# Performance work log

Measured on AMD Instinct MI355X. Metric: run time of the kernel, lower is better.

## Reference

```python
import jax, jax.numpy as jnp
import numpy as np

B, CIN, H, W = 32, 10, 128, 128
APP, WIDTH, M1, M2 = 2, 64, 20, 20
NQ, NP, OUT, MID = 4, 2, 1, 128
LIFT = WIDTH - CIN - APP - NQ  # 48


def setup_inputs() -> dict:
    key = jax.random.key(0)
    ks = jax.random.split(key, 16)
    n = lambda k, s: jax.random.normal(k, s, dtype=jnp.float32)
    sc = 1.0 / (WIDTH * WIDTH)  # FNO spectral weight scale 1/(in*out)
    return {
        'x': n(ks[0], (B, CIN, H, W)),
        'qa': n(ks[1], (NQ, CIN + APP)) * 0.1,
        'qb': n(ks[2], (NQ, CIN + APP)) * 0.1,
        'fc0_w1': n(ks[3], (MID, CIN + APP + NQ)) * 0.1,
        'fc0_b1': jnp.zeros((MID,), jnp.float32),
        'fc0_w2': n(ks[4], (LIFT, MID)) * 0.1,
        'fc0_b2': jnp.zeros((LIFT,), jnp.float32),
        'sw1r': n(ks[5], (4, WIDTH, WIDTH, M1, M2)) * sc,
        'sw1i': n(ks[6], (4, WIDTH, WIDTH, M1, M2)) * sc,
        'sw2r': n(ks[7], (4, WIDTH, WIDTH, M1, M2)) * sc,
        'sw2i': n(ks[8], (4, WIDTH, WIDTH, M1, M2)) * sc,
        'cw': n(ks[9], (4, WIDTH, WIDTH, 3, 3)) * 0.05,
        'cb': jnp.zeros((4, WIDTH), jnp.float32),
        'pw': n(ks[10], (4, WIDTH, 2 * WIDTH + NP)) * 0.05,
        'pb': jnp.zeros((4, WIDTH), jnp.float32),
        'fc1_w1': n(ks[11], (MID, WIDTH)) * 0.1,
        'fc1_b1': jnp.zeros((MID,), jnp.float32),
        'fc1_w2': n(ks[12], (OUT, MID)) * 0.1,
        'fc1_b2': jnp.zeros((OUT,), jnp.float32),
    }


def _conv1x1(x, w, b):
    # x: (B,C,H,W), w: (O,C), b: (O,)
    return jnp.einsum('oc,bchw->bohw', w, x) + b[None, :, None, None]


def _spectral_conv(x, w1, w2):
    # standard FNO2d spectral conv: keep low modes in both rfft corners
    xf = jnp.fft.rfft2(x)                                  # (B,C,H,W//2+1) complex
    top = jnp.einsum('bixy,ioxy->boxy', xf[:, :, :M1, :M2], w1)
    bot = jnp.einsum('bixy,ioxy->boxy', xf[:, :, -M1:, :M2], w2)
    of = jnp.zeros((x.shape[0], WIDTH, H, W // 2 + 1), dtype=xf.dtype)
    of = of.at[:, :, :M1, :M2].set(top).at[:, :, -M1:, :M2].set(bot)
    return jnp.fft.irfft2(of, s=(H, W))


def _circ_conv3(x, w, b):
    # Conv2d(k=3, padding=1, padding_mode='circular')
    xp = jnp.pad(x, ((0, 0), (0, 0), (1, 1), (1, 1)), mode='wrap')
    y = jax.lax.conv_general_dilated(xp, w, (1, 1), 'VALID',
                                     dimension_numbers=('NCHW', 'OIHW', 'NCHW'))
    return y + b[None, :, None, None]


def _grid(b, h, w):
    gx = jnp.broadcast_to(jnp.linspace(0.0, 1.0, h, dtype=jnp.float32)[None, None, :, None], (b, 1, h, w))
    gy = jnp.broadcast_to(jnp.linspace(0.0, 1.0, w, dtype=jnp.float32)[None, None, None, :], (b, 1, h, w))
    return jnp.concatenate([gx, gy], axis=1)


def reference(x, qa, qb, fc0_w1, fc0_b1, fc0_w2, fc0_b2,
              sw1r, sw1i, sw2r, sw2i, cw, cb, pw, pb,
              fc1_w1, fc1_b1, fc1_w2, fc1_b2):
    b = x.shape[0]
    x = jnp.concatenate([x, _grid(b, H, W)], axis=1)            # (B, 12, H, W)
    # QuadPath (prep stage): product of two learned linear projections
    q = jnp.einsum('oc,bchw->bohw', qa, x) * jnp.einsum('oc,bchw->bohw', qb, x)
    x = jnp.concatenate([x, q], axis=1)                          # (B, 16, H, W)
    # fc0 lift MLP (1x1 conv -> gelu -> 1x1 conv), concat to reach width
    h0 = jax.nn.gelu(_conv1x1(x, fc0_w1, fc0_b1))
    x = jnp.concatenate([x, _conv1x1(h0, fc0_w2, fc0_b2)], axis=1)  # (B, 64, H, W)

    for i in range(4):
        x1 = _spectral_conv(x, sw1r[i] + 1j * sw1i[i], sw2r[i] + 1j * sw2i[i])
        x2 = _circ_conv3(x, cw[i], cb[i])
        xo = jnp.concatenate([x1, x2], axis=1)                   # (B, 128, H, W)
        prods = xo[:, :NP] * xo[:, NP:2 * NP]                     # ProductLayer pair products
        xo = _conv1x1(jnp.concatenate([xo, prods], axis=1), pw[i], pb[i])
        x = x + jnp.tanh(xo)

    h1 = jax.nn.gelu(_conv1x1(x, fc1_w1, fc1_b1))
    return _conv1x1(h1, fc1_w2, fc1_b2)                          # (B, 1, H, W)
```

## Files before the change

### kernel.cpp

```cpp
#include <hip/hip_runtime.h>
#include <math.h>

#define HW 16384

typedef __attribute__((ext_vector_type(8))) short short8;
typedef __attribute__((ext_vector_type(4))) float f32x4;
typedef unsigned int u32;

__device__ __forceinline__ float gelu_tanh(float x) {
    float x3 = x * x * x;
    float t = tanhf(0.7978845608028654f * (x + 0.044715f * x3));
    return 0.5f * x * (1.0f + t);
}

__device__ __forceinline__ u32 f2bf(float f) {
    u32 u = __builtin_bit_cast(u32, f);
    return (u + 0x7FFFu + ((u >> 16) & 1u)) >> 16;
}
__device__ __forceinline__ u32 pack2(float a, float b) {
    return f2bf(a) | (f2bf(b) << 16);
}

__global__ __launch_bounds__(256) void packw_kernel(
    const float* __restrict__ cw, short* __restrict__ wpk)
{
    int idx = blockIdx.x * 256 + threadIdx.x;
    if (idx >= 4 * 64 * 576) return;
    int L = idx / 36864, r = idx % 36864;
    int o = r / 576, k = r % 576;
    int tap = k >> 6, i = k & 63;
    wpk[idx] = (short)f2bf(cw[((size_t)(L * 64 + o) * 64 + i) * 9 + tap]);
}
__global__ __launch_bounds__(256) void packpw_kernel(
    const float* __restrict__ pw, short* __restrict__ pwk)
{
    int idx = blockIdx.x * 256 + threadIdx.x;
    if (idx >= 4 * 64 * 128) return;
    int L = idx >> 13, r = idx & 8191;
    int o = r >> 7, k = r & 127;
    pwk[idx] = (short)f2bf(pw[(size_t)L * 8320 + o * 130 + k]);
}
__global__ __launch_bounds__(256) void packfc_kernel(
    const float* __restrict__ fc0w1, const float* __restrict__ fc0w2,
    const float* __restrict__ fc1w1,
    short* __restrict__ w1k, short* __restrict__ w2k, short* __restrict__ f1wk)
{
    int i = blockIdx.x * 256 + threadIdx.x;
    if (i < 4096) {
        int m = i >> 5, k = i & 31;
        w1k[i] = (short)(k < 16 ? f2bf(fc0w1[m * 16 + k]) : 0);
    } else if (i < 10240) {
        int j = i - 4096; int o = j >> 7, m = j & 127;
        w2k[j] = (short)f2bf(fc0w2[o * 128 + m]);
    } else if (i < 18432) {
        int j = i - 10240; int m = j >> 6, c = j & 63;
        f1wk[j] = (short)f2bf(fc1w1[m * 64 + c]);
    }
}
__global__ __launch_bounds__(256) void packsw_kernel(
    const float* __restrict__ sw1r, const float* __restrict__ sw1i,
    const float* __restrict__ sw2r, const float* __restrict__ sw2i,
    u32* __restrict__ wswk)
{
    __shared__ short lr[64][202];
    __shared__ short li[64][202];
    int bi = blockIdx.x;
    int L = bi >> 7, i = (bi >> 1) & 63, kh = bi & 1;
    int t = threadIdx.x;
    int km0 = kh * 200;
    for (int region = 0; region < 2; ++region) {
        const float* srcR = region ? sw2r : sw1r;
        const float* srcI = region ? sw2i : sw1i;
        size_t sb = ((size_t)(L * 64 + i) * 64) * 400 + km0;
        for (int c = 0; c < 50; ++c) {
            int flat = c * 256 + t;
            int o = flat / 200, km = flat - o * 200;
            lr[o][km] = (short)f2bf(srcR[sb + (size_t)o * 400 + km]);
            li[o][km] = (short)f2bf(srcI[sb + (size_t)o * 400 + km]);
        }
        __syncthreads();
        u32* dst = wswk + ((size_t)L * 800 + (size_t)region * 400 + km0) * 4096 + (size_t)i * 64;
        for (int c = 0; c < 50; ++c) {
            int flat = c * 256 + t;
            int km = flat >> 6, o = flat & 63;
            dst[(size_t)km * 4096 + o] =
                (u32)(unsigned short)lr[o][km] | ((u32)(unsigned short)li[o][km] << 16);
        }
        __syncthreads();
    }
}
__global__ __launch_bounds__(256) void gen_dft_kernel(
    short* __restrict__ Wfg, short* __restrict__ Winvbg,
    short* __restrict__ Tfy, short* __restrict__ Tiy)
{
    int idx = blockIdx.x * 256 + threadIdx.x;
    if (idx < 6144) {
        int n = idx >> 7, xx = idx & 127;
        float val = 0.f;
        if (n < 40) {
            int kx = n >> 1;
            float s, c;
            sincosf(6.283185307179586f * (float)((kx * xx) & 127) / 128.0f, &s, &c);
            val = (n & 1) ? -s : c;
        }
        Wfg[idx] = (short)f2bf(val);
    } else if (idx < 14336) {
        int j = idx - 6144;
        int xx = j >> 6, k = j & 63;
        float val = 0.f;
        if (k < 40) {
            int kx = k >> 1;
            if (kx == 0) {
                val = (k & 1) ? 0.f : (1.0f / 16384.0f);
            } else {
                float s, c;
                sincosf(6.283185307179586f * (float)((kx * xx) & 127) / 128.0f, &s, &c);
                val = ((k & 1) ? -s : c) * (2.0f / 16384.0f);
            }
        }
        Winvbg[j] = (short)f2bf(val);
    } else if (idx < 24576) {
        int j = idx - 14336;
        int q = j >> 7, yy = j & 127;
        int kyi = q >> 1;
        int ky = kyi + ((kyi >= 20) ? 88 : 0);
        float s, c;
        sincosf(6.283185307179586f * (float)((ky * yy) & 127) / 128.0f, &s, &c);
        Tfy[j] = (short)f2bf((q & 1) ? s : c);
    } else if (idx < 36864) {
        int j = idx - 24576;
        int yy = j / 96, q = j - yy * 96;
        float val = 0.f;
        if (q < 80) {
            int kyi = q >> 1;
            int ky = kyi + ((kyi >= 20) ? 88 : 0);
            float s, c;
            sincosf(6.283185307179586f * (float)((ky * yy) & 127) / 128.0f, &s, &c);
            val = (q & 1) ? s : c;
        }
        Tiy[j] = (short)f2bf(val);
    }
}

__global__ __launch_bounds__(256) void front_mfma_kernel(
    const float* __restrict__ x,
    const float* __restrict__ qa, const float* __restrict__ qb,
    const short* __restrict__ w1k, const float* __restrict__ b1,
    const short* __restrict__ w2k, const float* __restrict__ b2,
    float* __restrict__ xbuf, short* __restrict__ xb16)
{
    __shared__ short V[128 * 40];
    __shared__ short A2[128 * 136];
    __shared__ float lqa[48], lqb[48], lb1[128], lb2[48];
    int t = threadIdx.x;
    int y = blockIdx.x, b = blockIdx.y;
    int lane = t & 63, w = t >> 6;

    if (t < 48) { lqa[t] = qa[t]; lqb[t] = qb[t]; lb2[t] = b2[t]; }
    if (t >= 128) lb1[t - 128] = b1[t - 128];
    __syncthreads();

    if (t < 128) {
        int xx = t;
        float v[16];
        const float* xsrc = x + (size_t)b * 10 * HW + y * 128 + xx;
#pragma unroll
        for (int c = 0; c < 10; ++c) v[c] = xsrc[c * HW];
        v[10] = (float)y * (1.0f / 127.0f);
        v[11] = (float)xx * (1.0f / 127.0f);
#pragma unroll
        for (int o = 0; o < 4; ++o) {
            float sa = 0.f, sb = 0.f;
#pragma unroll
            for (int c = 0; c < 12; ++c) { sa += lqa[o * 12 + c] * v[c]; sb += lqb[o * 12 + c] * v[c]; }
            v[12 + o] = sa * sb;
        }
        u32* vr = (u32*)&V[xx * 40];
#pragma unroll
        for (int j = 0; j < 8; ++j) vr[j] = pack2(v[2 * j], v[2 * j + 1]);
#pragma unroll
        for (int j = 8; j < 16; ++j) vr[j] = 0u;
        float* ob = xbuf + (size_t)b * 64 * HW + y * 128 + xx;
#pragma unroll
        for (int c = 0; c < 16; ++c) ob[(size_t)c * HW] = v[c];
        u32* hb = (u32*)&xb16[(((size_t)b * 128 + y) * 128 + xx) * 64];
#pragma unroll
        for (int j = 0; j < 8; ++j) hb[j] = vr[j];
    }
    __syncthreads();

    {
        short8 aF[2];
#pragma unroll
        for (int mi = 0; mi < 2; ++mi)
            aF[mi] = *(const short8*)(w1k + ((w * 2 + mi) * 16 + (lane & 15)) * 32 + (lane >> 4) * 8);
        f32x4 acc[2][8];
#pragma unroll
        for (int mi = 0; mi < 2; ++mi)
#pragma unroll
            for (int nf = 0; nf < 8; ++nf) acc[mi][nf] = (f32x4){0.f, 0.f, 0.f, 0.f};
#pragma unroll
        for (int nf = 0; nf < 8; ++nf) {
            int xx = nf * 16 + (lane & 15);
            short8 bF = *(const short8*)&V[xx * 40 + (lane >> 4) * 8];
#pragma unroll
            for (int mi = 0; mi < 2; ++mi)
                acc[mi][nf] = __builtin_amdgcn_mfma_f32_16x16x32_bf16(aF[mi], bF, acc[mi][nf], 0, 0, 0);
        }
#pragma unroll
        for (int mi = 0; mi < 2; ++mi) {
            int m0 = (w * 2 + mi) * 16 + (lane >> 4) * 4;
            float bb0 = lb1[m0], bb1 = lb1[m0 + 1], bb2 = lb1[m0 + 2], bb3 = lb1[m0 + 3];
#pragma unroll
            for (int nf = 0; nf < 8; ++nf) {
                int xx = nf * 16 + (lane & 15);
                float h0 = gelu_tanh(acc[mi][nf][0] + bb0);
                float h1 = gelu_tanh(acc[mi][nf][1] + bb1);
                float h2 = gelu_tanh(acc[mi][nf][2] + bb2);
                float h3 = gelu_tanh(acc[mi][nf][3] + bb3);
                *(int2*)&A2[xx * 136 + m0] = make_int2(pack2(h0, h1), pack2(h2, h3));
            }
        }
    }
    __syncthreads();

    {
        short8 aF[3][4];
#pragma unroll
        for (int mt = 0; mt < 3; ++mt)
#pragma unroll
            for (int ks = 0; ks < 4; ++ks)
                aF[mt][ks] = *(const short8*)(w2k + (mt * 16 + (lane & 15)) * 128 + ks * 32 + (lane >> 4) * 8);
#pragma unroll
        for (int ni = 0; ni < 2; ++ni) {
            int nt = w * 2 + ni;
            int xx = nt * 16 + (lane & 15);
            f32x4 acc[3];
#pragma unroll
            for (int mt = 0; mt < 3; ++mt) acc[mt] = (f32x4){0.f, 0.f, 0.f, 0.f};
#pragma unroll
            for (int ks = 0; ks < 4; ++ks) {
                short8 bF = *(const short8*)&A2[xx * 136 + ks * 32 + (lane >> 4) * 8];
#pragma unroll
                for (int mt = 0; mt < 3; ++mt)
                    acc[mt] = __builtin_amdgcn_mfma_f32_16x16x32_bf16(aF[mt][ks], bF, acc[mt], 0, 0, 0);
            }
#pragma unroll
            for (int mt = 0; mt < 3; ++mt) {
                int o0 = mt * 16 + (lane >> 4) * 4;
                float r0 = acc[mt][0] + lb2[o0], r1 = acc[mt][1] + lb2[o0 + 1];
                float r2 = acc[mt][2] + lb2[o0 + 2], r3 = acc[mt][3] + lb2[o0 + 3];
                float* ob = xbuf + (size_t)b * 64 * HW + (size_t)(16 + o0) * HW + y * 128 + xx;
                ob[0] = r0; ob[HW] = r1; ob[2 * HW] = r2; ob[3 * HW] = r3;
                *(int2*)&xb16[(((size_t)b * 128 + y) * 128 + xx) * 64 + 16 + o0] =
                    make_int2(pack2(r0, r1), pack2(r2, r3));
            }
        }
    }
}

__global__ __launch_bounds__(256) void dftfwd_kernel(
    const float* __restrict__ xin, const short* __restrict__ Wfg,
    const short* __restrict__ Tfy, float2* __restrict__ fm)
{
    __shared__ short img[128 * 128];
    __shared__ short S[48 * 140];
    int t = threadIdx.x;
    int bc = blockIdx.x;
    int lane = t & 63, w = t >> 6;

    const float* src = xin + (size_t)bc * HW;
#pragma unroll
    for (int i = 0; i < 8; ++i) {
        int chunk = i * 256 + t;
        int y = chunk >> 4, x8 = chunk & 15;
        const float* p = src + y * 128 + x8 * 8;
        f32x4 v0 = *(const f32x4*)p, v1 = *(const f32x4*)(p + 4);
        int4 h = make_int4(pack2(v0[0], v0[1]), pack2(v0[2], v0[3]),
                           pack2(v1[0], v1[1]), pack2(v1[2], v1[3]));
        *(int4*)&img[y * 128 + ((x8 ^ (y & 7)) << 3)] = h;
    }
    for (int z = t; z < 560; z += 256) ((u32*)S)[2800 + z] = 0u;

    short8 bF[3][4];
#pragma unroll
    for (int nf = 0; nf < 3; ++nf)
#pragma unroll
        for (int ks = 0; ks < 4; ++ks) {
            int n = nf * 16 + (lane & 15);
            bF[nf][ks] = *(const short8*)(Wfg + n * 128 + ks * 32 + (lane >> 4) * 8);
        }
    __syncthreads();

    {
        f32x4 acc[2][3];
#pragma unroll
        for (int a = 0; a < 2; ++a)
#pragma unroll
            for (int b2 = 0; b2 < 3; ++b2) acc[a][b2] = (f32x4){0.f, 0.f, 0.f, 0.f};
#pragma unroll
        for (int ks = 0; ks < 4; ++ks)
#pragma unroll
            for (int mf = 0; mf < 2; ++mf) {
                int y = w * 32 + mf * 16 + (lane & 15);
                int x0 = ks * 32 + (lane >> 4) * 8;
                short8 aF = *(const short8*)&img[y * 128 + ((((x0 >> 3) ^ (y & 7))) << 3)];
#pragma unroll
                for (int nf = 0; nf < 3; ++nf)
                    acc[mf][nf] = __builtin_amdgcn_mfma_f32_16x16x32_bf16(aF, bF[nf][ks], acc[mf][nf], 0, 0, 0);
            }
#pragma unroll
        for (int mf = 0; mf < 2; ++mf)
#pragma unroll
            for (int nf = 0; nf < 3; ++nf) {
                int n = nf * 16 + (lane & 15);
                if (n < 40) {
                    int y0 = w * 32 + mf * 16 + (lane >> 4) * 4;
                    *(int2*)&S[n * 140 + y0] = make_int2(pack2(acc[mf][nf][0], acc[mf][nf][1]),
                                                         pack2(acc[mf][nf][2], acc[mf][nf][3]));
                }
            }
    }
    __syncthreads();

    float2* fmo = fm + (size_t)bc * 800;
#pragma unroll
    for (int pi = 0; pi < 4; ++pi) {
        int p = w + pi * 4;
        if (p < 15) {
            int mt = p / 3, nt = p % 3;
            f32x4 acc = (f32x4){0.f, 0.f, 0.f, 0.f};
#pragma unroll
            for (int ks = 0; ks < 4; ++ks) {
                short8 aF = *(const short8*)(Tfy + (mt * 16 + (lane & 15)) * 128 + ks * 32 + (lane >> 4) * 8);
                short8 bG = *(const short8*)&S[(nt * 16 + (lane & 15)) * 140 + ks * 32 + (lane >> 4) * 8];
                acc = __builtin_amdgcn_mfma_f32_16x16x32_bf16(aF, bG, acc, 0, 0, 0);
            }
            float p0 = __shfl_xor(acc[0], 1), p1 = __shfl_xor(acc[1], 1);
            float p2 = __shfl_xor(acc[2], 1), p3 = __shfl_xor(acc[3], 1);
            int l15 = lane & 15;
            if (!(l15 & 1)) {
                int kx = nt * 8 + (l15 >> 1);
                if (kx < 20) {
                    int kyi0 = mt * 8 + ((lane >> 4) << 1);
                    fmo[kyi0 * 20 + kx] = make_float2(acc[0] + p1, p0 - acc[1]);
                    fmo[(kyi0 + 1) * 20 + kx] = make_float2(acc[2] + p3, p2 - acc[3]);
                }
            }
        }
    }
}

__global__ __launch_bounds__(256) void specmul_kernel(
    const float2* __restrict__ fm,
    const u32* __restrict__ wswk,
    float2* __restrict__ fm2, int nb64)
{
    __shared__ float2 lx[32 * 64];
    __shared__ u32 lw[64 * 64];
    int t = threadIdx.x;
    int mode = blockIdx.x;
    const u32* ws = wswk + (size_t)mode * 4096;
    for (int n = t; n < nb64; n += 256)
        lx[n] = fm[(size_t)n * 800 + mode];
    for (int n = t; n < 4096; n += 256)
        lw[n] = ws[n];
    __syncthreads();
    for (int n = t; n < nb64; n += 256) {
        int b = n >> 6, o = n & 63;
        float re = 0.f, imv = 0.f;
        const float2* xb = lx + b * 64;
#pragma unroll 8
        for (int i = 0; i < 64; ++i) {
            float2 a = xb[i];
            u32 wp = lw[i * 64 + o];
            float wr = __builtin_bit_cast(float, wp << 16);
            float wi = __builtin_bit_cast(float, wp & 0xffff0000u);
            re += a.x * wr - a.y * wi;
            imv += a.x * wi + a.y * wr;
        }
        fm2[(size_t)n * 800 + mode] = make_float2(re, imv);
    }
}

__global__ __launch_bounds__(256) void invA_mfma_kernel(
    const float2* __restrict__ fm2, const short* __restrict__ Tiy,
    short* __restrict__ g)
{
    __shared__ short F[48 * 104];
    int t = threadIdx.x;
    int bc = blockIdx.x;
    int lane = t & 63, w = t >> 6;
    int bb = bc >> 6, cc = bc & 63;
    u32* Fw = (u32*)F;
    const float2* src = fm2 + (size_t)bc * 800;
    for (int i = t; i < 800; i += 256) {
        float2 v = src[i];
        int kyi = i / 20, kx = i - kyi * 20;
        Fw[(2 * kx) * 52 + kyi]     = pack2(v.x, -v.y);
        Fw[(2 * kx + 1) * 52 + kyi] = pack2(v.y, v.x);
    }
    for (int i = t; i < 416; i += 256) Fw[2080 + i] = 0u;
    for (int i = t; i < 384; i += 256) {
        int n = i >> 3, k = i & 7;
        Fw[n * 52 + 40 + k] = 0u;
    }
    __syncthreads();

    short8 aF[3][3];
#pragma unroll
    for (int mt = 0; mt < 3; ++mt)
#pragma unroll
        for (int ks = 0; ks < 3; ++ks)
            aF[mt][ks] = *(const short8*)&F[(mt * 16 + (lane & 15)) * 104 + ks * 32 + (lane >> 4) * 8];

#pragma unroll
    for (int ni = 0; ni < 2; ++ni) {
        int nt = w * 2 + ni;
        int yy = nt * 16 + (lane & 15);
        short8 bF[3];
#pragma unroll
        for (int ks = 0; ks < 3; ++ks)
            bF[ks] = *(const short8*)(Tiy + yy * 96 + ks * 32 + (lane >> 4) * 8);
#pragma unroll
        for (int mt = 0; mt < 3; ++mt) {
            f32x4 acc = (f32x4){0.f, 0.f, 0.f, 0.f};
#pragma unroll
            for (int ks = 0; ks < 3; ++ks)
                acc = __builtin_amdgcn_mfma_f32_16x16x32_bf16(aF[mt][ks], bF[ks], acc, 0, 0, 0);
            int n0 = mt * 16 + (lane >> 4) * 4;
            *(int2*)&g[(((size_t)bb * 128 + yy) * 64 + cc) * 48 + n0] =
                make_int2(pack2(acc[0], acc[1]), pack2(acc[2], acc[3]));
        }
    }
}

__global__ __launch_bounds__(256) void convcomb_kernel(
    const short* __restrict__ xb16o,
    const short* __restrict__ wpk,
    const float* __restrict__ cb,
    const short* __restrict__ g,
    const short* __restrict__ Winvbg,
    const short* __restrict__ pwk,
    const float* __restrict__ pw,
    const float* __restrict__ pb,
    float* __restrict__ xio,
    short* __restrict__ xb16n)
{
    __shared__ short xlds[3 * 128 * 64];
    __shared__ float2 pr[128];
    int t = threadIdx.x;
    int y = blockIdx.x;
    int b = blockIdx.y;
    int lane = t & 63, wid = t >> 6;
    short8 vz = {0, 0, 0, 0, 0, 0, 0, 0};

    const short8* xs = (const short8*)(xb16o + ((size_t)b * 128) * 128 * 64);
#pragma unroll
    for (int i = 0; i < 12; ++i) {
        int c = i * 256 + t;
        int row = c >> 10;
        int rem = c & 1023;
        int xx = rem >> 3, i8 = rem & 7;
        int yy = (y + row + 127) & 127;
        short8 v = xs[((size_t)yy * 128 + xx) * 8 + i8];
        *(short8*)&xlds[(row * 128 + xx) * 64 + ((i8 ^ (xx & 7)) << 3)] = v;
    }
    int o0 = wid * 16;
    const short* wbase = wpk + (size_t)(o0 + (lane & 15)) * 576 + (lane >> 4) * 8;
    short8 aFc[18];
#pragma unroll
    for (int s = 0; s < 18; ++s)
        aFc[s] = *(const short8*)(wbase + s * 32);
    short8 aG0, aG1;
    {
        const short* gb = g + ((size_t)(b * 128 + y)) * 64 * 48
                            + (size_t)(o0 + (lane & 15)) * 48;
        aG0 = *(const short8*)(gb + (lane >> 4) * 8);
        aG1 = ((lane >> 4) < 2) ? *(const short8*)(gb + 32 + (lane >> 4) * 8) : vz;
    }
    short8 bFi[8][2];
#pragma unroll
    for (int nf = 0; nf < 8; ++nf)
#pragma unroll
        for (int ks = 0; ks < 2; ++ks) {
            int xx = nf * 16 + (lane & 15);
            bFi[nf][ks] = *(const short8*)(Winvbg + xx * 64 + ks * 32 + (lane >> 4) * 8);
        }

    __syncthreads();

    f32x4 accC[8];
#pragma unroll
    for (int f = 0; f < 8; ++f) accC[f] = (f32x4){0.f, 0.f, 0.f, 0.f};
#pragma unroll
    for (int s = 0; s < 18; ++s) {
        const int tap = s >> 1;
        const int ky = tap / 3, kx = tap % 3;
        int ig = (s & 1) * 4 + (lane >> 4);
#pragma unroll
        for (int f = 0; f < 8; ++f) {
            int xx = (f * 16 + (lane & 15) + kx + 127) & 127;
            int off = (ky * 128 + xx) * 64 + ((ig ^ (xx & 7)) << 3);
            short8 bG = *(const short8*)&xlds[off];
            accC[f] = __builtin_amdgcn_mfma_f32_16x16x32_bf16(aFc[s], bG, accC[f], 0, 0, 0);
        }
    }
    f32x4 accI[8];
#pragma unroll
    for (int nf = 0; nf < 8; ++nf) {
        f32x4 acc = (f32x4){0.f, 0.f, 0.f, 0.f};
        acc = __builtin_amdgcn_mfma_f32_16x16x32_bf16(aG0, bFi[nf][0], acc, 0, 0, 0);
        acc = __builtin_amdgcn_mfma_f32_16x16x32_bf16(aG1, bFi[nf][1], acc, 0, 0, 0);
        accI[nf] = acc;
    }

    __syncthreads();

    short* S1 = xlds;
    short* C2 = xlds + 8192;
    {
        int cw = o0 + (lane >> 4) * 4;
        int swg = (cw >> 3) & 7;
        int cwo = cw & 7;
        bool dopr = (wid == 0) && ((lane >> 4) == 0);
#pragma unroll
        for (int nf = 0; nf < 8; ++nf) {
            int xx = nf * 16 + (lane & 15);
            int dst = xx * 64 + ((swg ^ (xx & 7)) << 3) + cwo;
            *(int2*)&S1[dst] = make_int2(pack2(accI[nf][0], accI[nf][1]),
                                         pack2(accI[nf][2], accI[nf][3]));
            if (dopr) pr[xx] = make_float2(accI[nf][0] * accI[nf][2],
                                           accI[nf][1] * accI[nf][3]);
        }
        float bias0 = cb[cw], bias1 = cb[cw + 1], bias2 = cb[cw + 2], bias3 = cb[cw + 3];
#pragma unroll
        for (int f = 0; f < 8; ++f) {
            int xx = f * 16 + (lane & 15);
            int dst = xx * 64 + ((swg ^ (xx & 7)) << 3) + cwo;
            *(int2*)&C2[dst] = make_int2(pack2(accC[f][0] + bias0, accC[f][1] + bias1),
                                         pack2(accC[f][2] + bias2, accC[f][3] + bias3));
        }
    }
    short8 bFp[4][4];
#pragma unroll
    for (int nf = 0; nf < 4; ++nf)
#pragma unroll
        for (int ks = 0; ks < 4; ++ks) {
            int o = nf * 16 + (lane & 15);
            bFp[nf][ks] = *(const short8*)(pwk + o * 128 + ks * 32 + (lane >> 4) * 8);
        }
    __syncthreads();

    f32x4 acc[2][4];
#pragma unroll
    for (int a = 0; a < 2; ++a)
#pragma unroll
        for (int b2 = 0; b2 < 4; ++b2) acc[a][b2] = (f32x4){0.f, 0.f, 0.f, 0.f};

#pragma unroll
    for (int ks = 0; ks < 4; ++ks)
#pragma unroll
        for (int mf = 0; mf < 2; ++mf) {
            int xx = wid * 32 + mf * 16 + (lane & 15);
            int k0 = ks * 32 + (lane >> 4) * 8;
            const short* src = (ks < 2) ? &S1[xx * 64 + ((((k0 >> 3) ^ (xx & 7))) << 3)]
                                        : &C2[xx * 64 + (((((k0 - 64) >> 3) ^ (xx & 7))) << 3)];
            short8 aF = *(const short8*)src;
#pragma unroll
            for (int nf = 0; nf < 4; ++nf)
                acc[mf][nf] = __builtin_amdgcn_mfma_f32_16x16x32_bf16(aF, bFp[nf][ks], acc[mf][nf], 0, 0, 0);
        }

#pragma unroll
    for (int mf = 0; mf < 2; ++mf) {
        int xr = wid * 32 + mf * 16 + (lane >> 4) * 4;
        float2 prv0 = pr[xr], prv1 = pr[xr + 1], prv2 = pr[xr + 2], prv3 = pr[xr + 3];
#pragma unroll
        for (int nf = 0; nf < 4; ++nf) {
            int o = nf * 16 + (lane & 15);
            const float* pwrow = pw + o * 130;
            float pw128 = pwrow[128], pw129 = pwrow[129], pbv = pb[o];
            size_t off = ((size_t)(b * 64 + o)) * HW + y * 128 + xr;
            f32x4 xov = *(const f32x4*)(xio + off);
            f32x4 res;
            res[0] = xov[0] + tanhf(acc[mf][nf][0] + pbv + pw128 * prv0.x + pw129 * prv0.y);
            res[1] = xov[1] + tanhf(acc[mf][nf][1] + pbv + pw128 * prv1.x + pw129 * prv1.y);
            res[2] = xov[2] + tanhf(acc[mf][nf][2] + pbv + pw128 * prv2.x + pw129 * prv2.y);
            res[3] = xov[3] + tanhf(acc[mf][nf][3] + pbv + pw128 * prv3.x + pw129 * prv3.y);
            *(f32x4*)(xio + off) = res;
            size_t hbase = (((size_t)(b * 128 + y)) * 128 + xr) * 64 + o;
            xb16n[hbase]       = (short)f2bf(res[0]);
            xb16n[hbase + 64]  = (short)f2bf(res[1]);
            xb16n[hbase + 128] = (short)f2bf(res[2]);
            xb16n[hbase + 192] = (short)f2bf(res[3]);
        }
    }
}

__global__ __launch_bounds__(256) void fc1_mfma_kernel(
    const short* __restrict__ xb16,
    const short* __restrict__ f1wk, const float* __restrict__ b1,
    const float* __restrict__ w2, const float* __restrict__ b2,
    float* __restrict__ out)
{
    __shared__ short X[128 * 72];
    __shared__ float lb1[128], lw2[128];
    int t = threadIdx.x;
    int y = blockIdx.x, b = blockIdx.y;
    int lane = t & 63, w = t >> 6;
    if (t < 128) { lb1[t] = b1[t]; lw2[t] = w2[t]; }
    const short8* src = (const short8*)(xb16 + (((size_t)b * 128 + y) * 128) * 64);
#pragma unroll
    for (int i = 0; i < 4; ++i) {
        int c = i * 256 + t;
        int xx = c >> 3, c8 = c & 7;
        *(short8*)&X[xx * 72 + ((c8 ^ (xx & 7)) << 3)] = src[c];
    }
    __syncthreads();

    float part0 = 0.f, part1 = 0.f;
#pragma unroll
    for (int mt = 0; mt < 8; ++mt) {
        short8 aF[2];
#pragma unroll
        for (int ks = 0; ks < 2; ++ks)
            aF[ks] = *(const short8*)(f1wk + (mt * 16 + (lane & 15)) * 64 + ks * 32 + (lane >> 4) * 8);
#pragma unroll
        for (int ni = 0; ni < 2; ++ni) {
            int xx = (w * 2 + ni) * 16 + (lane & 15);
            f32x4 acc = (f32x4){0.f, 0.f, 0.f, 0.f};
#pragma unroll
            for (int ks = 0; ks < 2; ++ks) {
                int g8 = ks * 4 + (lane >> 4);
                short8 bF = *(const short8*)&X[xx * 72 + ((g8 ^ (xx & 7)) << 3)];
                acc = __builtin_amdgcn_mfma_f32_16x16x32_bf16(aF[ks], bF, acc, 0, 0, 0);
            }
            int m0 = mt * 16 + (lane >> 4) * 4;
            float s = lw2[m0]     * gelu_tanh(acc[0] + lb1[m0])
                    + lw2[m0 + 1] * gelu_tanh(acc[1] + lb1[m0 + 1])
                    + lw2[m0 + 2] * gelu_tanh(acc[2] + lb1[m0 + 2])
                    + lw2[m0 + 3] * gelu_tanh(acc[3] + lb1[m0 + 3]);
            if (ni == 0) part0 += s; else part1 += s;
        }
    }
    part0 += __shfl_xor(part0, 16); part0 += __shfl_xor(part0, 32);
    part1 += __shfl_xor(part1, 16); part1 += __shfl_xor(part1, 32);
    if (lane < 16) {
        float bb = b2[0];
        out[(size_t)b * HW + y * 128 + (w * 2) * 16 + lane] = part0 + bb;
        out[(size_t)b * HW + y * 128 + (w * 2 + 1) * 16 + lane] = part1 + bb;
    }
}

extern "C" void kernel_launch(void* const* d_in, const int* in_sizes, int n_in,
                              void* d_out, int out_size, void* d_ws, size_t ws_size,
                              hipStream_t stream) {
    const float* x      = (const float*)d_in[0];
    const float* qa     = (const float*)d_in[1];
    const float* qb     = (const float*)d_in[2];
    const float* fc0w1  = (const float*)d_in[3];
    const float* fc0b1  = (const float*)d_in[4];
    const float* fc0w2  = (const float*)d_in[5];
    const float* fc0b2  = (const float*)d_in[6];
    const float* sw1r   = (const float*)d_in[7];
    const float* sw1i   = (const float*)d_in[8];
    const float* sw2r   = (const float*)d_in[9];
    const float* sw2i   = (const float*)d_in[10];
    const float* cw     = (const float*)d_in[11];
    const float* cb     = (const float*)d_in[12];
    const float* pw     = (const float*)d_in[13];
    const float* pb     = (const float*)d_in[14];
    const float* fc1w1  = (const float*)d_in[15];
    const float* fc1b1  = (const float*)d_in[16];
    const float* fc1w2  = (const float*)d_in[17];
    const float* fc1b2  = (const float*)d_in[18];

    const size_t WPK_F = 73728, PWK_F = 16384, WFG_F = 3072, WIB_F = 4096;
    const size_t TFY_F = 5120, TIY_F = 6144, FCK_F = 9216;
    const size_t WSW_F = 13107200;
    const size_t CONST_F = WPK_F + PWK_F + WFG_F + WIB_F + TFY_F + TIY_F + FCK_F + WSW_F;
    const size_t PER_B_F = 1048576u + 2u * 524288u + 196608u + 2u * 102400u;
    int NB = 32;
    while (NB > 1 && ((size_t)NB * PER_B_F + CONST_F) * 4 > ws_size) NB >>= 1;
    if (((size_t)NB * PER_B_F + CONST_F) * 4 > ws_size) return;

    float* fb = (float*)d_ws;
    short* wpk    = (short*)fb;                 fb += WPK_F;
    short* pwk    = (short*)fb;                 fb += PWK_F;
    short* Wfg    = (short*)fb;                 fb += WFG_F;
    short* Winvbg = (short*)fb;                 fb += WIB_F;
    short* Tfy    = (short*)fb;                 fb += TFY_F;
    short* Tiy    = (short*)fb;                 fb += TIY_F;
    short* w1k    = (short*)fb;
    short* w2k    = w1k + 4096;
    short* f1wk   = w1k + 10240;                fb += FCK_F;
    u32*   wswk   = (u32*)fb;                   fb += WSW_F;

    float*  xA    = fb;
    short*  xb16A = (short*)(xA + (size_t)NB * 1048576u);
    short*  xb16B = xb16A + (size_t)NB * 1048576u;
    short*  g     = xb16B + (size_t)NB * 1048576u;
    float2* fm    = (float2*)(g + (size_t)NB * 393216u);
    float2* fm2   = fm + (size_t)NB * 51200u;

    packw_kernel<<<576, 256, 0, stream>>>(cw, wpk);
    packpw_kernel<<<128, 256, 0, stream>>>(pw, pwk);
    packfc_kernel<<<72, 256, 0, stream>>>(fc0w1, fc0w2, fc1w1, w1k, w2k, f1wk);
    gen_dft_kernel<<<144, 256, 0, stream>>>(Wfg, Winvbg, Tfy, Tiy);
    packsw_kernel<<<512, 256, 0, stream>>>(sw1r, sw1i, sw2r, sw2i, wswk);

    for (int b0 = 0; b0 < 32; b0 += NB) {
        front_mfma_kernel<<<dim3(128, NB), 256, 0, stream>>>(
            x + (size_t)b0 * 10 * HW, qa, qb, w1k, fc0b1, w2k, fc0b2, xA, xb16A);

        short* xo = xb16A;
        short* xn = xb16B;
        for (int L = 0; L < 4; ++L) {
            dftfwd_kernel<<<NB * 64, 256, 0, stream>>>(xA, Wfg, Tfy, fm);
            specmul_kernel<<<800, 256, 0, stream>>>(fm, wswk + (size_t)L * 800 * 4096,
                                                    fm2, NB * 64);
            invA_mfma_kernel<<<NB * 64, 256, 0, stream>>>(fm2, Tiy, g);
            convcomb_kernel<<<dim3(128, NB), 256, 0, stream>>>(
                xo, wpk + (size_t)L * 36864, cb + (size_t)L * 64,
                g, Winvbg, pwk + (size_t)L * 8192, pw + (size_t)L * 8320,
                pb + (size_t)L * 64, xA, xn);
            short* tmp = xo; xo = xn; xn = tmp;
        }

        fc1_mfma_kernel<<<dim3(128, NB), 256, 0, stream>>>(
            xo, f1wk, fc1b1, fc1w2, fc1b2, (float*)d_out + (size_t)b0 * HW);
    }
}
```

Before: 1.453 ms.

## Split convcomb rows into half-width tiles and make specmul write in place

The conv+combine kernel now processes half a row (64 columns plus a 1-column halo on each side) per block, with twice as many blocks. This cuts LDS use from about 48KB to about 25KB and halves the per-thread accumulator arrays, so occupancy should rise. The cost is re-reading the halo columns and the shared weights once per half. The spectral multiply also writes its result back into the input buffer rather than a separate fm2 buffer, which saves workspace. That in-place write is safe because each block reads all of its inputs into LDS before writing.

```diff
diff --git a/kernel.cpp b/kernel.cpp
--- a/kernel.cpp
+++ b/kernel.cpp
@@ -352,9 +352,8 @@
 }
 
 __global__ __launch_bounds__(256) void specmul_kernel(
-    const float2* __restrict__ fm,
-    const u32* __restrict__ wswk,
-    float2* __restrict__ fm2, int nb64)
+    float2* __restrict__ fm,
+    const u32* __restrict__ wswk, int nb64)
 {
     __shared__ float2 lx[32 * 64];
     __shared__ u32 lw[64 * 64];
@@ -379,12 +378,12 @@
             re += a.x * wr - a.y * wi;
             imv += a.x * wi + a.y * wr;
         }
-        fm2[(size_t)n * 800 + mode] = make_float2(re, imv);
+        fm[(size_t)n * 800 + mode] = make_float2(re, imv);
     }
 }
 
 __global__ __launch_bounds__(256) void invA_mfma_kernel(
-    const float2* __restrict__ fm2, const short* __restrict__ Tiy,
+    const float2* __restrict__ fm, const short* __restrict__ Tiy,
     short* __restrict__ g)
 {
     __shared__ short F[48 * 104];
@@ -393,7 +392,7 @@
     int lane = t & 63, w = t >> 6;
     int bb = bc >> 6, cc = bc & 63;
     u32* Fw = (u32*)F;
-    const float2* src = fm2 + (size_t)bc * 800;
+    const float2* src = fm + (size_t)bc * 800;
     for (int i = t; i < 800; i += 256) {
         float2 v = src[i];
         int kyi = i / 20, kx = i - kyi * 20;
@@ -447,24 +446,29 @@
     float* __restrict__ xio,
     short* __restrict__ xb16n)
 {
-    __shared__ short xlds[3 * 128 * 64];
-    __shared__ float2 pr[128];
+    __shared__ short xlds[3 * 66 * 64];
+    __shared__ float2 pr[64];
     int t = threadIdx.x;
-    int y = blockIdx.x;
+    int bx = blockIdx.x;
+    int y = bx >> 1, h = bx & 1;
     int b = blockIdx.y;
     int lane = t & 63, wid = t >> 6;
     short8 vz = {0, 0, 0, 0, 0, 0, 0, 0};
 
     const short8* xs = (const short8*)(xb16o + ((size_t)b * 128) * 128 * 64);
-#pragma unroll
-    for (int i = 0; i < 12; ++i) {
+    int xbase = h * 64 - 1;
+#pragma unroll
+    for (int i = 0; i < 7; ++i) {
         int c = i * 256 + t;
-        int row = c >> 10;
-        int rem = c & 1023;
-        int xx = rem >> 3, i8 = rem & 7;
-        int yy = (y + row + 127) & 127;
-        short8 v = xs[((size_t)yy * 128 + xx) * 8 + i8];
-        *(short8*)&xlds[(row * 128 + xx) * 64 + ((i8 ^ (xx & 7)) << 3)] = v;
+        if (c < 1584) {
+            int row = c / 528;
+            int rem = c - row * 528;
+            int xl = rem >> 3, i8 = rem & 7;
+            int yy = (y + row + 127) & 127;
+            int xg = (xbase + xl + 128) & 127;
+            short8 v = xs[((size_t)yy * 128 + xg) * 8 + i8];
+            *(short8*)&xlds[(row * 66 + xl) * 64 + ((i8 ^ (xl & 7)) << 3)] = v;
+        }
     }
     int o0 = wid * 16;
     const short* wbase = wpk + (size_t)(o0 + (lane & 15)) * 576 + (lane >> 4) * 8;
@@ -479,36 +483,36 @@
         aG0 = *(const short8*)(gb + (lane >> 4) * 8);
         aG1 = ((lane >> 4) < 2) ? *(const short8*)(gb + 32 + (lane >> 4) * 8) : vz;
     }
-    short8 bFi[8][2];
-#pragma unroll
-    for (int nf = 0; nf < 8; ++nf)
+    short8 bFi[4][2];
+#pragma unroll
+    for (int nf = 0; nf < 4; ++nf)
 #pragma unroll
         for (int ks = 0; ks < 2; ++ks) {
-            int xx = nf * 16 + (lane & 15);
-            bFi[nf][ks] = *(const short8*)(Winvbg + xx * 64 + ks * 32 + (lane >> 4) * 8);
-        }
-
-    __syncthreads();
-
-    f32x4 accC[8];
-#pragma unroll
-    for (int f = 0; f < 8; ++f) accC[f] = (f32x4){0.f, 0.f, 0.f, 0.f};
+            int xxg = h * 64 + nf * 16 + (lane & 15);
+            bFi[nf][ks] = *(const short8*)(Winvbg + xxg * 64 + ks * 32 + (lane >> 4) * 8);
+        }
+
+    __syncthreads();
+
+    f32x4 accC[4];
+#pragma unroll
+    for (int f = 0; f < 4; ++f) accC[f] = (f32x4){0.f, 0.f, 0.f, 0.f};
 #pragma unroll
     for (int s = 0; s < 18; ++s) {
         const int tap = s >> 1;
         const int ky = tap / 3, kx = tap % 3;
         int ig = (s & 1) * 4 + (lane >> 4);
 #pragma unroll
-        for (int f = 0; f < 8; ++f) {
-            int xx = (f * 16 + (lane & 15) + kx + 127) & 127;
-            int off = (ky * 128 + xx) * 64 + ((ig ^ (xx & 7)) << 3);
+        for (int f = 0; f < 4; ++f) {
+            int xin = f * 16 + (lane & 15) + kx;
+            int off = (ky * 66 + xin) * 64 + ((ig ^ (xin & 7)) << 3);
             short8 bG = *(const short8*)&xlds[off];
             accC[f] = __builtin_amdgcn_mfma_f32_16x16x32_bf16(aFc[s], bG, accC[f], 0, 0, 0);
         }
     }
-    f32x4 accI[8];
-#pragma unroll
-    for (int nf = 0; nf < 8; ++nf) {
+    f32x4 accI[4];
+#pragma unroll
+    for (int nf = 0; nf < 4; ++nf) {
         f32x4 acc = (f32x4){0.f, 0.f, 0.f, 0.f};
         acc = __builtin_amdgcn_mfma_f32_16x16x32_bf16(aG0, bFi[nf][0], acc, 0, 0, 0);
         acc = __builtin_amdgcn_mfma_f32_16x16x32_bf16(aG1, bFi[nf][1], acc, 0, 0, 0);
@@ -518,26 +522,26 @@
     __syncthreads();
 
     short* S1 = xlds;
-    short* C2 = xlds + 8192;
+    short* C2 = xlds + 4096;
     {
         int cw = o0 + (lane >> 4) * 4;
         int swg = (cw >> 3) & 7;
         int cwo = cw & 7;
         bool dopr = (wid == 0) && ((lane >> 4) == 0);
 #pragma unroll
-        for (int nf = 0; nf < 8; ++nf) {
-            int xx = nf * 16 + (lane & 15);
-            int dst = xx * 64 + ((swg ^ (xx & 7)) << 3) + cwo;
+        for (int nf = 0; nf < 4; ++nf) {
+            int xl = nf * 16 + (lane & 15);
+            int dst = xl * 64 + ((swg ^ (xl & 7)) << 3) + cwo;
             *(int2*)&S1[dst] = make_int2(pack2(accI[nf][0], accI[nf][1]),
                                          pack2(accI[nf][2], accI[nf][3]));
-            if (dopr) pr[xx] = make_float2(accI[nf][0] * accI[nf][2],
+            if (dopr) pr[xl] = make_float2(accI[nf][0] * accI[nf][2],
                                            accI[nf][1] * accI[nf][3]);
         }
         float bias0 = cb[cw], bias1 = cb[cw + 1], bias2 = cb[cw + 2], bias3 = cb[cw + 3];
 #pragma unroll
-        for (int f = 0; f < 8; ++f) {
-            int xx = f * 16 + (lane & 15);
-            int dst = xx * 64 + ((swg ^ (xx & 7)) << 3) + cwo;
+        for (int f = 0; f < 4; ++f) {
+            int xl = f * 16 + (lane & 15);
+            int dst = xl * 64 + ((swg ^ (xl & 7)) << 3) + cwo;
             *(int2*)&C2[dst] = make_int2(pack2(accC[f][0] + bias0, accC[f][1] + bias1),
                                          pack2(accC[f][2] + bias2, accC[f][3] + bias3));
         }
@@ -552,44 +556,39 @@
         }
     __syncthreads();
 
-    f32x4 acc[2][4];
-#pragma unroll
-    for (int a = 0; a < 2; ++a)
-#pragma unroll
-        for (int b2 = 0; b2 < 4; ++b2) acc[a][b2] = (f32x4){0.f, 0.f, 0.f, 0.f};
-
-#pragma unroll
-    for (int ks = 0; ks < 4; ++ks)
-#pragma unroll
-        for (int mf = 0; mf < 2; ++mf) {
-            int xx = wid * 32 + mf * 16 + (lane & 15);
-            int k0 = ks * 32 + (lane >> 4) * 8;
-            const short* src = (ks < 2) ? &S1[xx * 64 + ((((k0 >> 3) ^ (xx & 7))) << 3)]
-                                        : &C2[xx * 64 + (((((k0 - 64) >> 3) ^ (xx & 7))) << 3)];
-            short8 aF = *(const short8*)src;
-#pragma unroll
-            for (int nf = 0; nf < 4; ++nf)
-                acc[mf][nf] = __builtin_amdgcn_mfma_f32_16x16x32_bf16(aF, bFp[nf][ks], acc[mf][nf], 0, 0, 0);
-        }
-
-#pragma unroll
-    for (int mf = 0; mf < 2; ++mf) {
-        int xr = wid * 32 + mf * 16 + (lane >> 4) * 4;
+    f32x4 acc[4];
+#pragma unroll
+    for (int nf = 0; nf < 4; ++nf) acc[nf] = (f32x4){0.f, 0.f, 0.f, 0.f};
+    int xxl = wid * 16 + (lane & 15);
+#pragma unroll
+    for (int ks = 0; ks < 4; ++ks) {
+        int k0 = ks * 32 + (lane >> 4) * 8;
+        const short* srcp = (ks < 2) ? &S1[xxl * 64 + ((((k0 >> 3) ^ (xxl & 7))) << 3)]
+                                     : &C2[xxl * 64 + (((((k0 - 64) >> 3) ^ (xxl & 7))) << 3)];
+        short8 aF = *(const short8*)srcp;
+#pragma unroll
+        for (int nf = 0; nf < 4; ++nf)
+            acc[nf] = __builtin_amdgcn_mfma_f32_16x16x32_bf16(aF, bFp[nf][ks], acc[nf], 0, 0, 0);
+    }
+
+    {
+        int xr = wid * 16 + (lane >> 4) * 4;
+        int xg2 = h * 64 + xr;
         float2 prv0 = pr[xr], prv1 = pr[xr + 1], prv2 = pr[xr + 2], prv3 = pr[xr + 3];
 #pragma unroll
         for (int nf = 0; nf < 4; ++nf) {
             int o = nf * 16 + (lane & 15);
             const float* pwrow = pw + o * 130;
             float pw128 = pwrow[128], pw129 = pwrow[129], pbv = pb[o];
-            size_t off = ((size_t)(b * 64 + o)) * HW + y * 128 + xr;
+            size_t off = ((size_t)(b * 64 + o)) * HW + y * 128 + xg2;
             f32x4 xov = *(const f32x4*)(xio + off);
             f32x4 res;
-            res[0] = xov[0] + tanhf(acc[mf][nf][0] + pbv + pw128 * prv0.x + pw129 * prv0.y);
-            res[1] = xov[1] + tanhf(acc[mf][nf][1] + pbv + pw128 * prv1.x + pw129 * prv1.y);
-            res[2] = xov[2] + tanhf(acc[mf][nf][2] + pbv + pw128 * prv2.x + pw129 * prv2.y);
-            res[3] = xov[3] + tanhf(acc[mf][nf][3] + pbv + pw128 * prv3.x + pw129 * prv3.y);
+            res[0] = xov[0] + tanhf(acc[nf][0] + pbv + pw128 * prv0.x + pw129 * prv0.y);
+            res[1] = xov[1] + tanhf(acc[nf][1] + pbv + pw128 * prv1.x + pw129 * prv1.y);
+            res[2] = xov[2] + tanhf(acc[nf][2] + pbv + pw128 * prv2.x + pw129 * prv2.y);
+            res[3] = xov[3] + tanhf(acc[nf][3] + pbv + pw128 * prv3.x + pw129 * prv3.y);
             *(f32x4*)(xio + off) = res;
-            size_t hbase = (((size_t)(b * 128 + y)) * 128 + xr) * 64 + o;
+            size_t hbase = (((size_t)(b * 128 + y)) * 128 + xg2) * 64 + o;
             xb16n[hbase]       = (short)f2bf(res[0]);
             xb16n[hbase + 64]  = (short)f2bf(res[1]);
             xb16n[hbase + 128] = (short)f2bf(res[2]);
@@ -680,7 +679,7 @@
     const size_t TFY_F = 5120, TIY_F = 6144, FCK_F = 9216;
     const size_t WSW_F = 13107200;
     const size_t CONST_F = WPK_F + PWK_F + WFG_F + WIB_F + TFY_F + TIY_F + FCK_F + WSW_F;
-    const size_t PER_B_F = 1048576u + 2u * 524288u + 196608u + 2u * 102400u;
+    const size_t PER_B_F = 1048576u + 2u * 524288u + 196608u + 102400u;
     int NB = 32;
     while (NB > 1 && ((size_t)NB * PER_B_F + CONST_F) * 4 > ws_size) NB >>= 1;
     if (((size_t)NB * PER_B_F + CONST_F) * 4 > ws_size) return;
@@ -702,7 +701,6 @@
     short*  xb16B = xb16A + (size_t)NB * 1048576u;
     short*  g     = xb16B + (size_t)NB * 1048576u;
     float2* fm    = (float2*)(g + (size_t)NB * 393216u);
-    float2* fm2   = fm + (size_t)NB * 51200u;
 
     packw_kernel<<<576, 256, 0, stream>>>(cw, wpk);
     packpw_kernel<<<128, 256, 0, stream>>>(pw, pwk);
@@ -719,9 +717,9 @@
         for (int L = 0; L < 4; ++L) {
             dftfwd_kernel<<<NB * 64, 256, 0, stream>>>(xA, Wfg, Tfy, fm);
             specmul_kernel<<<800, 256, 0, stream>>>(fm, wswk + (size_t)L * 800 * 4096,
-                                                    fm2, NB * 64);
-            invA_mfma_kernel<<<NB * 64, 256, 0, stream>>>(fm2, Tiy, g);
-            convcomb_kernel<<<dim3(128, NB), 256, 0, stream>>>(
+                                                    NB * 64);
+            invA_mfma_kernel<<<NB * 64, 256, 0, stream>>>(fm, Tiy, g);
+            convcomb_kernel<<<dim3(256, NB), 256, 0, stream>>>(
                 xo, wpk + (size_t)L * 36864, cb + (size_t)L * 64,
                 g, Winvbg, pwk + (size_t)L * 8192, pw + (size_t)L * 8320,
                 pb + (size_t)L * 64, xA, xn);
```

New measurement: 1.616 ms. +11.2%, slower.
